# Performance work log

Measured on AMD Instinct MI355X. Metric: run time of the kernel, lower is better.

Reference implementation:

```python
import jax, jax.numpy as jnp
import numpy as np

B, N, D, NS, HID = 256, 1024, 64, 8, 128
ITERS, SINK_ITERS, MESH_ITERS = 3, 8, 4
MESH_LR = 3.0
EPS = 1e-8


def _grid():
    # build_coords with latent_resolution=(32,32): meshgrid('xy'), flattened to [1024,2]
    x = np.linspace(0.0, 1.0, 32)
    xv, yv = np.meshgrid(x, x)
    g = np.stack([xv.reshape(-1), yv.reshape(-1)], axis=-1)
    return jnp.asarray(g, dtype=jnp.float32)


def layer_norm(x, g, b):
    m = jnp.mean(x, axis=-1, keepdims=True)
    v = jnp.var(x, axis=-1, keepdims=True)
    return (x - m) * jax.lax.rsqrt(v + 1e-5) * g + b


def cdist(k, q):
    # Euclidean pairwise distance: k [b,n,d], q [b,s,d] -> [b,n,s]
    d2 = (jnp.sum(k * k, -1)[..., :, None] + jnp.sum(q * q, -1)[..., None, :]
          - 2.0 * jnp.einsum('bnd,bsd->bns', k, q))
    return jnp.sqrt(jnp.maximum(d2, 1e-12))


def sinkhorn(C, a, b, u=None, v=None, n_iters=SINK_ITERS):
    # log-domain Sinkhorn; C [b,n,s], row marginal a [b,n], col marginal b [b,s]
    log_a = jnp.log(a + EPS)
    log_b = jnp.log(b + EPS)
    if u is None:
        u = jnp.zeros_like(a)
    if v is None:
        v = jnp.zeros_like(b)
    K = -C

    def body(carry, _):
        u, v = carry
        u = log_a - jax.scipy.special.logsumexp(K + v[..., None, :], axis=-1)
        v = log_b - jax.scipy.special.logsumexp(K + u[..., :, None], axis=-2)
        return (u, v), None

    (u, v), _ = jax.lax.scan(body, (u, v), None, length=n_iters)
    P = jnp.exp(K + u[..., :, None] + v[..., None, :])
    return P, u, v


def minimize_entropy_of_sinkhorn(C0, a, b, mesh_lr=MESH_LR, n_mesh_iters=MESH_ITERS):
    # MESH: gradient descent on the cost matrix to minimize Sinkhorn plan entropy
    def ent(C):
        P, u, v = sinkhorn(C, a, b)
        H = -jnp.sum(P * jnp.log(P + EPS))
        return H, (u, v)

    C = C0
    u = v = None
    for _ in range(n_mesh_iters):
        (_, (u, v)), g = jax.value_and_grad(ent, has_aux=True)(C)
        C = C - mesh_lr * g
    return C, u, v


def gru_cell(x, h, w_ih, w_hh, b_ih, b_hh):
    gi = x @ w_ih.T + b_ih
    gh = h @ w_hh.T + b_hh
    i_r, i_z, i_n = jnp.split(gi, 3, axis=-1)
    h_r, h_z, h_n = jnp.split(gh, 3, axis=-1)
    r = jax.nn.sigmoid(i_r + h_r)
    z = jax.nn.sigmoid(i_z + h_z)
    n = jnp.tanh(i_n + r * h_n)
    return (1.0 - z) * n + z * h


def setup_inputs() -> dict:
    key = jax.random.key(0)
    ks = jax.random.split(key, 16)
    s = D ** -0.5
    inp = {
        'inputs': jax.random.normal(ks[0], (B, N, D), jnp.float32),
        'noise': jax.random.normal(ks[1], (B, NS, D), jnp.float32),
        'slots_mu': jax.random.normal(ks[2], (1, 1, D), jnp.float32),
        'slots_sigma': jax.random.uniform(ks[3], (1, 1, D), jnp.float32),
        'Wq': jax.random.normal(ks[4], (D, D), jnp.float32) * s,
        'Wk': jax.random.normal(ks[5], (D, D), jnp.float32) * s,
        'Wv': jax.random.normal(ks[6], (D, D), jnp.float32) * s,
        'gru_w_ih': jax.random.normal(ks[7], (3 * D, D), jnp.float32) * s,
        'gru_w_hh': jax.random.normal(ks[8], (3 * D, D), jnp.float32) * s,
        'gru_b_ih': jnp.zeros((3 * D,), jnp.float32),
        'gru_b_hh': jnp.zeros((3 * D,), jnp.float32),
        'fc1_w': jax.random.normal(ks[9], (HID, D), jnp.float32) * s,
        'fc1_b': jnp.zeros((HID,), jnp.float32),
        'fc2_w': jax.random.normal(ks[10], (D, HID), jnp.float32) * (HID ** -0.5),
        'fc2_b': jnp.zeros((D,), jnp.float32),
        'ln_in_g': jnp.ones((D,), jnp.float32), 'ln_in_b': jnp.zeros((D,), jnp.float32),
        'ln_slots_g': jnp.ones((D,), jnp.float32), 'ln_slots_b': jnp.zeros((D,), jnp.float32),
        'ln_ff_g': jnp.ones((D,), jnp.float32), 'ln_ff_b': jnp.zeros((D,), jnp.float32),
        'wi_w': jax.random.normal(ks[11], (1, D), jnp.float32) * s,
        'wi_b': jnp.zeros((1,), jnp.float32),
        'ws_w': jax.random.normal(ks[12], (1, D), jnp.float32) * s,
        'ws_b': jnp.zeros((1,), jnp.float32),
    }
    return inp


def _forward(inputs, noise, slots_mu, slots_sigma, Wq, Wk, Wv,
             gru_w_ih, gru_w_hh, gru_b_ih, gru_b_hh,
             fc1_w, fc1_b, fc2_w, fc2_b,
             ln_in_g, ln_in_b, ln_slots_g, ln_slots_b, ln_ff_g, ln_ff_b,
             wi_w, wi_b, ws_w, ws_b):
    b_s, n, d = inputs.shape
    n_s = NS
    # slots ~ Normal(mu, |sigma|+eps) via reparameterized noise
    slots = slots_mu + (jnp.abs(slots_sigma) + EPS) * noise  # [b, n_s, d]

    x = layer_norm(inputs, ln_in_g, ln_in_b)
    k = x @ Wk.T
    v = x @ Wv.T
    grid = _grid()  # [N, 2]
    a = jax.nn.softmax((x @ wi_w.T + wi_b)[..., 0], axis=-1) * n_s  # [b, n]

    for _ in range(ITERS):
        slots_prev = slots
        s_n = layer_norm(slots, ln_slots_g, ln_slots_b)
        bm = jax.nn.softmax((s_n @ ws_w.T + ws_b)[..., 0], axis=-1) * n_s  # [b, n_s]
        q = s_n @ Wq.T
        C = cdist(k, q)  # [b, n, n_s]
        C, p, qq = minimize_entropy_of_sinkhorn(C, a, bm)
        attn, _, _ = sinkhorn(C, a, bm, u=p, v=qq)
        attn = jnp.transpose(attn, (0, 2, 1))  # [b, n_s, n]
        updates = attn @ v  # [b, n_s, d]
        slot_pos = jnp.einsum('bqk,kd->bqd', attn, grid)  # [b, n_s, 2]
        slots = gru_cell(updates.reshape(b_s * n_s, d),
                         slots_prev.reshape(b_s * n_s, d),
                         gru_w_ih, gru_w_hh, gru_b_ih, gru_b_hh).reshape(b_s, n_s, d)
        slots = slots + (jax.nn.relu(layer_norm(slots, ln_ff_g, ln_ff_b) @ fc1_w.T + fc1_b) @ fc2_w.T + fc2_b)
    return slots, slot_pos.reshape(b_s, n_s, 2), attn


def reference(inputs, noise, slots_mu, slots_sigma, Wq, Wk, Wv,
              gru_w_ih, gru_w_hh, gru_b_ih, gru_b_hh,
              fc1_w, fc1_b, fc2_w, fc2_b,
              ln_in_g, ln_in_b, ln_slots_g, ln_slots_b, ln_ff_g, ln_ff_b,
              wi_w, wi_b, ws_w, ws_b):
    return _forward(inputs, noise, slots_mu, slots_sigma, Wq, Wk, Wv,
                    gru_w_ih, gru_w_hh, gru_b_ih, gru_b_hh,
                    fc1_w, fc1_b, fc2_w, fc2_b,
                    ln_in_g, ln_in_b, ln_slots_g, ln_slots_b, ln_ff_g, ln_ff_b,
                    wi_w, wi_b, ws_w, ws_b)
```

## Files before the change

### kernel.cpp

```cpp
#include <hip/hip_runtime.h>
#include <math.h>

#define NB   256
#define NN   1024
#define ND   64
#define NSL  8
#define NHID 128
#define N_SINK 8
#define N_MESH 4
#define F_LR  3.0f
#define F_EPS 1e-8f

__global__ __launch_bounds__(256) void k_pre(
    const float* __restrict__ inp, const float* __restrict__ Wk,
    const float* __restrict__ lng, const float* __restrict__ lnb,
    const float* __restrict__ wiw, const float* __restrict__ wib,
    float* __restrict__ xout, float* __restrict__ kkout, float* __restrict__ wilog) {
  __shared__ __align__(16) float xs[4][64];
  int wv = threadIdx.x >> 6, ln = threadIdx.x & 63;
  size_t row = (size_t)blockIdx.x * 4 + wv;
  float xi = inp[row * 64 + ln];
  float s1 = xi, s2 = xi * xi;
  #pragma unroll
  for (int m = 32; m >= 1; m >>= 1) { s1 += __shfl_xor(s1, m, 64); s2 += __shfl_xor(s2, m, 64); }
  float mean = s1 * (1.f / 64.f);
  float var  = s2 * (1.f / 64.f) - mean * mean;
  float xn = (xi - mean) * rsqrtf(var + 1e-5f) * lng[ln] + lnb[ln];
  xs[wv][ln] = xn;
  xout[row * 64 + ln] = xn;
  float wl = xn * wiw[ln];
  #pragma unroll
  for (int m = 32; m >= 1; m >>= 1) wl += __shfl_xor(wl, m, 64);
  __syncthreads();
  const float4* w4 = (const float4*)(Wk + ln * 64);
  const float4* x4 = (const float4*)xs[wv];
  float ko = 0.f;
  #pragma unroll
  for (int c = 0; c < 16; ++c) {
    float4 a = w4[c], xv = x4[c];
    ko += a.x * xv.x + a.y * xv.y + a.z * xv.z + a.w * xv.w;
  }
  float kk = ko * ko;
  #pragma unroll
  for (int m = 32; m >= 1; m >>= 1) kk += __shfl_xor(kk, m, 64);
  if (ln == 0) { kkout[row] = kk; wilog[row] = wl + wib[0]; }
}

__global__ __launch_bounds__(1024, 4) void k_mega(
    const float* __restrict__ noise, const float* __restrict__ mu,
    const float* __restrict__ sigma,
    const float* __restrict__ xg, const float* __restrict__ kkg,
    const float* __restrict__ wilogg,
    const float* __restrict__ Wq, const float* __restrict__ Wk,
    const float* __restrict__ Wv,
    const float* __restrict__ wih, const float* __restrict__ whh,
    const float* __restrict__ bih, const float* __restrict__ bhh,
    const float* __restrict__ fc1w, const float* __restrict__ fc1b,
    const float* __restrict__ fc2w, const float* __restrict__ fc2b,
    const float* __restrict__ lns_g, const float* __restrict__ lns_b,
    const float* __restrict__ lnf_g, const float* __restrict__ lnf_b,
    const float* __restrict__ wsw, const float* __restrict__ wsb,
    float* __restrict__ out_slots, float* __restrict__ out_pos,
    float* __restrict__ out_attn) {
  __shared__ __align__(16) float slot_lds[8][64];
  __shared__ __align__(16) float sn[8][64];
  __shared__ __align__(16) float qsh[8][64];
  __shared__ __align__(16) float qs[8][64];
  __shared__ __align__(16) float updl[8][64];
  __shared__ __align__(16) float ys[8][64];
  __shared__ __align__(16) float rs[8][128];
  __shared__ __align__(16) union {
    float uhist[N_SINK][NN];
    float part[16][8][64];
  } U;
  __shared__ __align__(16) float cols[8][NN];
  __shared__ float vbc[8];
  __shared__ float vbarbc[8];
  __shared__ float vhist[N_SINK][8];
  __shared__ float bmv[8], q2s[8], lbs[8];
  __shared__ float redf[16], bcf[1];

  int b = blockIdx.x, tid = threadIdx.x;
  int wv = tid >> 6, ln = tid & 63;

  if (tid < 512) {
    slot_lds[tid >> 6][ln] = mu[ln] + (fabsf(sigma[ln]) + F_EPS) * noise[(size_t)b * 512 + tid];
  }
  float wl = wilogg[(size_t)b * NN + tid];
  float m0 = wl;
  #pragma unroll
  for (int s = 32; s >= 1; s >>= 1) m0 = fmaxf(m0, __shfl_xor(m0, s, 64));
  if (ln == 0) redf[wv] = m0;
  __syncthreads();
  if (tid == 0) { float a = redf[0]; for (int w = 1; w < 16; ++w) a = fmaxf(a, redf[w]); bcf[0] = a; }
  __syncthreads();
  m0 = bcf[0];
  float e0 = __expf(wl - m0), se0 = e0;
  #pragma unroll
  for (int s = 32; s >= 1; s >>= 1) se0 += __shfl_xor(se0, s, 64);
  __syncthreads();
  if (ln == 0) redf[wv] = se0;
  __syncthreads();
  if (tid == 0) { float a = 0.f; for (int w = 0; w < 16; ++w) a += redf[w]; bcf[0] = a; }
  __syncthreads();
  float la = __logf(8.f * e0 / bcf[0] + F_EPS);
  float kk = kkg[(size_t)b * NN + tid];
  const float4* xrow4 = (const float4*)(xg + ((size_t)b * NN + tid) * ND);

  float u = 0.f;

  for (int it = 0; it < 3; ++it) {
    if (wv < 8) {
      float x = slot_lds[wv][ln];
      float s1 = x, s2 = x * x;
      #pragma unroll
      for (int m = 32; m >= 1; m >>= 1) { s1 += __shfl_xor(s1, m, 64); s2 += __shfl_xor(s2, m, 64); }
      float mean = s1 * (1.f / 64.f);
      float var  = s2 * (1.f / 64.f) - mean * mean;
      float xn = (x - mean) * rsqrtf(var + 1e-5f) * lns_g[ln] + lns_b[ln];
      sn[wv][ln] = xn;
      float wlg = xn * wsw[ln];
      #pragma unroll
      for (int m = 32; m >= 1; m >>= 1) wlg += __shfl_xor(wlg, m, 64);
      if (ln == 0) bmv[wv] = wlg + wsb[0];
    }
    __syncthreads();
    if (wv < 8) {
      const float4* w4 = (const float4*)(Wq + ln * 64);
      const float4* x4 = (const float4*)sn[wv];
      float q = 0.f;
      #pragma unroll
      for (int c = 0; c < 16; ++c) {
        float4 a = w4[c], xv = x4[c];
        q += a.x * xv.x + a.y * xv.y + a.z * xv.z + a.w * xv.w;
      }
      qsh[wv][ln] = q;
      float q2 = q * q;
      #pragma unroll
      for (int m = 32; m >= 1; m >>= 1) q2 += __shfl_xor(q2, m, 64);
      if (ln == 0) q2s[wv] = q2;
    }
    if (tid >= 512 && tid < 520) {
      int j = tid - 512;
      float mx = bmv[0];
      #pragma unroll
      for (int jj = 1; jj < 8; ++jj) mx = fmaxf(mx, bmv[jj]);
      float ss = 0.f;
      #pragma unroll
      for (int jj = 0; jj < 8; ++jj) ss += __expf(bmv[jj] - mx);
      lbs[j] = __logf(8.f * __expf(bmv[j] - mx) / ss + F_EPS);
    }
    __syncthreads();
    if (wv < 8) {
      float qt = 0.f;
      for (int o = 0; o < 64; ++o) qt = fmaf(qsh[wv][o], Wk[o * 64 + ln], qt);
      qs[wv][ln] = qt;
    }
    __syncthreads();

    float Know[8];
    {
      float dot[8];
      #pragma unroll
      for (int j = 0; j < 8; ++j) dot[j] = 0.f;
      #pragma unroll 4
      for (int c = 0; c < 16; ++c) {
        float4 xv = xrow4[c];
        #pragma unroll
        for (int j = 0; j < 8; ++j) {
          const float4 qv = *(const float4*)&qs[j][c * 4];
          dot[j] += xv.x * qv.x + xv.y * qv.y + xv.z * qv.z + xv.w * qv.w;
        }
      }
      #pragma unroll
      for (int j = 0; j < 8; ++j) {
        float d2 = kk + q2s[j] - 2.f * dot[j];
        Know[j] = -sqrtf(fmaxf(d2, 1e-12f));
      }
    }
    for (int phase = 0; phase <= N_MESH; ++phase) {
      bool cold = (phase < N_MESH);
      for (int t = 0; t < N_SINK; ++t) {
        bool z0 = cold && (t == 0);
        float c0[8];
        #pragma unroll
        for (int j = 0; j < 8; ++j) c0[j] = Know[j] + (z0 ? 0.f : vbc[j]);
        float mx = c0[0];
        #pragma unroll
        for (int j = 1; j < 8; ++j) mx = fmaxf(mx, c0[j]);
        float se = 0.f;
        #pragma unroll
        for (int j = 0; j < 8; ++j) se += __expf(c0[j] - mx);
        u = la - (mx + __logf(se));
        U.uhist[t][tid] = u;
        #pragma unroll
        for (int j = 0; j < 8; ++j) cols[j][tid] = Know[j] + u;
        __syncthreads();
        if (wv < 8) {
          const float* cp = &cols[wv][ln];
          float M = cp[0];
          #pragma unroll
          for (int k = 1; k < 16; ++k) M = fmaxf(M, cp[k * 64]);
          #pragma unroll
          for (int d = 32; d >= 1; d >>= 1) M = fmaxf(M, __shfl_xor(M, d, 64));
          float S = 0.f;
          #pragma unroll
          for (int k = 0; k < 16; ++k) S += __expf(cp[k * 64] - M);
          #pragma unroll
          for (int d = 32; d >= 1; d >>= 1) S += __shfl_xor(S, d, 64);
          if (ln == 0) {
            float vj = lbs[wv] - (M + __logf(S));
            vbc[wv] = vj; vhist[t][wv] = vj;
          }
        }
        __syncthreads();
      }
      if (phase == N_MESH) break;

      float Kbar[8], ubarT;
      {
        float gsum = 0.f;
        #pragma unroll
        for (int j = 0; j < 8; ++j) {
          float P  = __expf(Know[j] + u + vbc[j]);
          float pe = P + F_EPS;
          float G  = -(__logf(pe) + P / pe);
          float gp = G * P;
          Kbar[j] = gp; gsum += gp;
          cols[j][tid] = gp;
        }
        ubarT = gsum;
      }
      __syncthreads();
      if (wv < 8) {
        const float* cp = &cols[wv][ln];
        float S = 0.f;
        #pragma unroll
        for (int k = 0; k < 16; ++k) S += cp[k * 64];
        #pragma unroll
        for (int d = 32; d >= 1; d >>= 1) S += __shfl_xor(S, d, 64);
        if (ln == 0) vbarbc[wv] = S;
      }
      __syncthreads();
      for (int t = N_SINK - 1; t >= 0; --t) {
        float ut = U.uhist[t][tid];
        float dsum = (t == N_SINK - 1) ? ubarT : 0.f;
        #pragma unroll
        for (int j = 0; j < 8; ++j) {
          float w  = __expf(Know[j] + ut + vhist[t][j] - lbs[j]);
          float vw = vbarbc[j] * w;
          Kbar[j] -= vw; dsum -= vw;
        }
        #pragma unroll
        for (int j = 0; j < 8; ++j) {
          float vprev = (t > 0) ? vhist[t - 1][j] : 0.f;
          float z  = __expf(Know[j] + vprev + ut - la);
          float uz = dsum * z;
          Kbar[j] -= uz;
          cols[j][tid] = uz;
        }
        if (t > 0) {
          __syncthreads();
          if (wv < 8) {
            const float* cp = &cols[wv][ln];
            float S = 0.f;
            #pragma unroll
            for (int k = 0; k < 16; ++k) S += cp[k * 64];
            #pragma unroll
            for (int d = 32; d >= 1; d >>= 1) S += __shfl_xor(S, d, 64);
            if (ln == 0) vbarbc[wv] = -S;
          }
          __syncthreads();
        }
      }
      #pragma unroll
      for (int j = 0; j < 8; ++j) Know[j] -= F_LR * Kbar[j];
    }
    #pragma unroll
    for (int j = 0; j < 8; ++j) {
      float P = __expf(Know[j] + u + vbc[j]);
      cols[j][tid] = P;
      if (it == 2) out_attn[((size_t)b * 8 + j) * NN + tid] = P;
    }
    __syncthreads();

    {
      float acc[8];
      #pragma unroll
      for (int j = 0; j < 8; ++j) acc[j] = 0.f;
      const float* xc = xg + ((size_t)b * NN + wv * 64) * ND + ln;
      #pragma unroll 2
      for (int i0 = 0; i0 < 64; i0 += 4) {
        float x0 = xc[(size_t)(i0 + 0) * 64];
        float x1 = xc[(size_t)(i0 + 1) * 64];
        float x2 = xc[(size_t)(i0 + 2) * 64];
        float x3 = xc[(size_t)(i0 + 3) * 64];
        int ir = wv * 64 + i0;
        #pragma unroll
        for (int j = 0; j < 8; ++j) {
          float4 a = *(const float4*)&cols[j][ir];
          acc[j] += a.x * x0 + a.y * x1 + a.z * x2 + a.w * x3;
        }
      }
      #pragma unroll
      for (int j = 0; j < 8; ++j) U.part[wv][j][ln] = acc[j];
    }
    if (it == 2 && wv < 8) {
      float px = 0.f, py = 0.f;
      #pragma unroll
      for (int k = 0; k < 16; ++k) {
        int i = ln + k * 64;
        float a = cols[wv][i];
        px += a * (float)(i & 31);
        py += a * (float)(i >> 5);
      }
      #pragma unroll
      for (int m = 32; m >= 1; m >>= 1) { px += __shfl_xor(px, m, 64); py += __shfl_xor(py, m, 64); }
      if (ln == 0) {
        out_pos[(b * 8 + wv) * 2 + 0] = px * (1.f / 31.f);
        out_pos[(b * 8 + wv) * 2 + 1] = py * (1.f / 31.f);
      }
    }
    __syncthreads();
    if (wv < 8) {
      float s = 0.f;
      #pragma unroll
      for (int w = 0; w < 16; ++w) s += U.part[w][wv][ln];
      updl[wv][ln] = s;
    }
    __syncthreads();
    if (wv < 8) {
      const float4* w4 = (const float4*)(Wv + ln * 64);
      const float4* u4 = (const float4*)updl[wv];
      float updv = 0.f;
      #pragma unroll
      for (int c = 0; c < 16; ++c) {
        float4 uv = u4[c], wvv = w4[c];
        updv += uv.x * wvv.x + uv.y * wvv.y + uv.z * wvv.z + uv.w * wvv.w;
      }
      sn[wv][ln] = updv;
    }
    __syncthreads();

    float hn = 0.f;
    if (wv < 8) {
      float h = slot_lds[wv][ln];
      float gi0 = bih[ln], gi1 = bih[64 + ln], gi2 = bih[128 + ln];
      float gh0 = bhh[ln], gh1 = bhh[64 + ln], gh2 = bhh[128 + ln];
      const float4* x4 = (const float4*)sn[wv];
      const float4* h4 = (const float4*)slot_lds[wv];
      const float4* wi0 = (const float4*)(wih + (size_t)ln * 64);
      const float4* wi1 = (const float4*)(wih + (size_t)(64 + ln) * 64);
      const float4* wi2 = (const float4*)(wih + (size_t)(128 + ln) * 64);
      const float4* wh0 = (const float4*)(whh + (size_t)ln * 64);
      const float4* wh1 = (const float4*)(whh + (size_t)(64 + ln) * 64);
      const float4* wh2 = (const float4*)(whh + (size_t)(128 + ln) * 64);
      #pragma unroll 4
      for (int c = 0; c < 16; ++c) {
        float4 xv = x4[c], hv = h4[c], a;
        a = wi0[c]; gi0 += xv.x * a.x + xv.y * a.y + xv.z * a.z + xv.w * a.w;
        a = wi1[c]; gi1 += xv.x * a.x + xv.y * a.y + xv.z * a.z + xv.w * a.w;
        a = wi2[c]; gi2 += xv.x * a.x + xv.y * a.y + xv.z * a.z + xv.w * a.w;
        a = wh0[c]; gh0 += hv.x * a.x + hv.y * a.y + hv.z * a.z + hv.w * a.w;
        a = wh1[c]; gh1 += hv.x * a.x + hv.y * a.y + hv.z * a.z + hv.w * a.w;
        a = wh2[c]; gh2 += hv.x * a.x + hv.y * a.y + hv.z * a.z + hv.w * a.w;
      }
      float r = 1.f / (1.f + expf(-(gi0 + gh0)));
      float z = 1.f / (1.f + expf(-(gi1 + gh1)));
      float n = tanhf(gi2 + r * gh2);
      hn = (1.f - z) * n + z * h;
      float s1 = hn, s2 = hn * hn;
      #pragma unroll
      for (int m = 32; m >= 1; m >>= 1) { s1 += __shfl_xor(s1, m, 64); s2 += __shfl_xor(s2, m, 64); }
      float mean = s1 * (1.f / 64.f);
      float var  = s2 * (1.f / 64.f) - mean * mean;
      ys[wv][ln] = (hn - mean) * rsqrtf(var + 1e-5f) * lnf_g[ln] + lnf_b[ln];
    }
    __syncthreads();
    if (wv < 8) {
      float a0 = fc1b[ln], a1 = fc1b[64 + ln];
      const float4* y4 = (const float4*)ys[wv];
      const float4* f0 = (const float4*)(fc1w + (size_t)ln * 64);
      const float4* f1 = (const float4*)(fc1w + (size_t)(64 + ln) * 64);
      #pragma unroll 4
      for (int c = 0; c < 16; ++c) {
        float4 yv = y4[c], a = f0[c], bb = f1[c];
        a0 += yv.x * a.x + yv.y * a.y + yv.z * a.z + yv.w * a.w;
        a1 += yv.x * bb.x + yv.y * bb.y + yv.z * bb.z + yv.w * bb.w;
      }
      rs[wv][ln] = fmaxf(a0, 0.f);
      rs[wv][64 + ln] = fmaxf(a1, 0.f);
    }
    __syncthreads();
    if (wv < 8) {
      float o = fc2b[ln];
      const float4* r4 = (const float4*)rs[wv];
      const float4* f2 = (const float4*)(fc2w + (size_t)ln * 128);
      #pragma unroll 4
      for (int c = 0; c < 32; ++c) {
        float4 rv = r4[c], a = f2[c];
        o += rv.x * a.x + rv.y * a.y + rv.z * a.z + rv.w * a.w;
      }
      slot_lds[wv][ln] = hn + o;
    }
    __syncthreads();
  }
  if (tid < 512) out_slots[(size_t)b * 512 + tid] = slot_lds[tid >> 6][ln];
}

extern "C" void kernel_launch(void* const* d_in, const int* in_sizes, int n_in,
                              void* d_out, int out_size, void* d_ws, size_t ws_size,
                              hipStream_t stream) {
  const float* inputs = (const float*)d_in[0];
  const float* noise  = (const float*)d_in[1];
  const float* mu     = (const float*)d_in[2];
  const float* sigma  = (const float*)d_in[3];
  const float* Wq     = (const float*)d_in[4];
  const float* Wk     = (const float*)d_in[5];
  const float* Wv     = (const float*)d_in[6];
  const float* gwih   = (const float*)d_in[7];
  const float* gwhh   = (const float*)d_in[8];
  const float* gbih   = (const float*)d_in[9];
  const float* gbhh   = (const float*)d_in[10];
  const float* fc1w   = (const float*)d_in[11];
  const float* fc1b   = (const float*)d_in[12];
  const float* fc2w   = (const float*)d_in[13];
  const float* fc2b   = (const float*)d_in[14];
  const float* lnin_g = (const float*)d_in[15];
  const float* lnin_b = (const float*)d_in[16];
  const float* lns_g  = (const float*)d_in[17];
  const float* lns_b  = (const float*)d_in[18];
  const float* lnf_g  = (const float*)d_in[19];
  const float* lnf_b  = (const float*)d_in[20];
  const float* wi_w   = (const float*)d_in[21];
  const float* wi_b   = (const float*)d_in[22];
  const float* ws_w   = (const float*)d_in[23];
  const float* ws_b   = (const float*)d_in[24];

  float* out       = (float*)d_out;
  float* out_slots = out;
  float* out_pos   = out + NB * NSL * ND;
  float* out_attn  = out_pos + NB * NSL * 2;

  float* p = (float*)d_ws;
  float* xbuf  = p; p += (size_t)NB * NN * ND;
  float* kkbuf = p; p += (size_t)NB * NN;
  float* wilog = p; p += (size_t)NB * NN;

  k_pre<<<(NB * NN) / 4, 256, 0, stream>>>(inputs, Wk, lnin_g, lnin_b, wi_w, wi_b,
                                           xbuf, kkbuf, wilog);
  k_mega<<<NB, 1024, 0, stream>>>(noise, mu, sigma, xbuf, kkbuf, wilog,
                                  Wq, Wk, Wv, gwih, gwhh, gbih, gbhh,
                                  fc1w, fc1b, fc2w, fc2b,
                                  lns_g, lns_b, lnf_g, lnf_b, ws_w, ws_b,
                                  out_slots, out_pos, out_attn);
}
```

Measured before the change: 1.330 ms.

## Keep cost matrix in LDS and recompute column terms instead of staging cols

The per-thread Know[8] register array becomes a shared-memory cost matrix, and the separate cols staging buffer is removed. Column reductions now recompute their terms (the exp and log expressions) directly from know, uhist, dsum and la held in LDS, which also drops one barrier in the mesh backward step. The launch-bounds occupancy hint is relaxed and several unroll factors are reduced to lower register pressure. The cost is extra transcendental recomputation in the wave-limited column reductions and LDS reads in place of register reads.

After: 1.317 ms. Within noise of the previous version (-1.0%).

```diff
diff --git a/kernel.cpp b/kernel.cpp
--- a/kernel.cpp
+++ b/kernel.cpp
@@ -46,7 +46,7 @@
   if (ln == 0) { kkout[row] = kk; wilog[row] = wl + wib[0]; }
 }
 
-__global__ __launch_bounds__(1024, 4) void k_mega(
+__global__ __launch_bounds__(1024) void k_mega(
     const float* __restrict__ noise, const float* __restrict__ mu,
     const float* __restrict__ sigma,
     const float* __restrict__ xg, const float* __restrict__ kkg,
@@ -62,6 +62,13 @@
     const float* __restrict__ wsw, const float* __restrict__ wsb,
     float* __restrict__ out_slots, float* __restrict__ out_pos,
     float* __restrict__ out_attn) {
+  __shared__ __align__(16) float know[8][NN];
+  __shared__ __align__(16) union {
+    float uhist[N_SINK][NN];
+    float part[16][8][64];
+  } U;
+  __shared__ __align__(16) float dsb[NN];
+  __shared__ __align__(16) float la_lds[NN];
   __shared__ __align__(16) float slot_lds[8][64];
   __shared__ __align__(16) float sn[8][64];
   __shared__ __align__(16) float qsh[8][64];
@@ -69,11 +76,6 @@
   __shared__ __align__(16) float updl[8][64];
   __shared__ __align__(16) float ys[8][64];
   __shared__ __align__(16) float rs[8][128];
-  __shared__ __align__(16) union {
-    float uhist[N_SINK][NN];
-    float part[16][8][64];
-  } U;
-  __shared__ __align__(16) float cols[8][NN];
   __shared__ float vbc[8];
   __shared__ float vbarbc[8];
   __shared__ float vhist[N_SINK][8];
@@ -104,6 +106,7 @@
   if (tid == 0) { float a = 0.f; for (int w = 0; w < 16; ++w) a += redf[w]; bcf[0] = a; }
   __syncthreads();
   float la = __logf(8.f * e0 / bcf[0] + F_EPS);
+  la_lds[tid] = la;
   float kk = kkg[(size_t)b * NN + tid];
   const float4* xrow4 = (const float4*)(xg + ((size_t)b * NN + tid) * ND);
 
@@ -158,7 +161,6 @@
     }
     __syncthreads();
 
-    float Know[8];
     {
       float dot[8];
       #pragma unroll
@@ -175,37 +177,37 @@
       #pragma unroll
       for (int j = 0; j < 8; ++j) {
         float d2 = kk + q2s[j] - 2.f * dot[j];
-        Know[j] = -sqrtf(fmaxf(d2, 1e-12f));
+        know[j][tid] = -sqrtf(fmaxf(d2, 1e-12f));
       }
     }
     for (int phase = 0; phase <= N_MESH; ++phase) {
       bool cold = (phase < N_MESH);
       for (int t = 0; t < N_SINK; ++t) {
         bool z0 = cold && (t == 0);
-        float c0[8];
-        #pragma unroll
-        for (int j = 0; j < 8; ++j) c0[j] = Know[j] + (z0 ? 0.f : vbc[j]);
-        float mx = c0[0];
-        #pragma unroll
-        for (int j = 1; j < 8; ++j) mx = fmaxf(mx, c0[j]);
+        float kv[8];
+        #pragma unroll
+        for (int j = 0; j < 8; ++j) kv[j] = know[j][tid] + (z0 ? 0.f : vbc[j]);
+        float mx = kv[0];
+        #pragma unroll
+        for (int j = 1; j < 8; ++j) mx = fmaxf(mx, kv[j]);
         float se = 0.f;
         #pragma unroll
-        for (int j = 0; j < 8; ++j) se += __expf(c0[j] - mx);
+        for (int j = 0; j < 8; ++j) se += __expf(kv[j] - mx);
         u = la - (mx + __logf(se));
         U.uhist[t][tid] = u;
-        #pragma unroll
-        for (int j = 0; j < 8; ++j) cols[j][tid] = Know[j] + u;
         __syncthreads();
         if (wv < 8) {
-          const float* cp = &cols[wv][ln];
-          float M = cp[0];
+          float tv[16];
           #pragma unroll
-          for (int k = 1; k < 16; ++k) M = fmaxf(M, cp[k * 64]);
+          for (int k = 0; k < 16; ++k) tv[k] = know[wv][ln + k * 64] + U.uhist[t][ln + k * 64];
+          float M = tv[0];
+          #pragma unroll
+          for (int k = 1; k < 16; ++k) M = fmaxf(M, tv[k]);
           #pragma unroll
           for (int d = 32; d >= 1; d >>= 1) M = fmaxf(M, __shfl_xor(M, d, 64));
           float S = 0.f;
           #pragma unroll
-          for (int k = 0; k < 16; ++k) S += __expf(cp[k * 64] - M);
+          for (int k = 0; k < 16; ++k) S += __expf(tv[k] - M);
           #pragma unroll
           for (int d = 32; d >= 1; d >>= 1) S += __shfl_xor(S, d, 64);
           if (ln == 0) {
@@ -222,21 +224,23 @@
         float gsum = 0.f;
         #pragma unroll
         for (int j = 0; j < 8; ++j) {
-          float P  = __expf(Know[j] + u + vbc[j]);
+          float P  = __expf(know[j][tid] + u + vbc[j]);
           float pe = P + F_EPS;
-          float G  = -(__logf(pe) + P / pe);
-          float gp = G * P;
+          float gp = -(__logf(pe) + P / pe) * P;
           Kbar[j] = gp; gsum += gp;
-          cols[j][tid] = gp;
         }
         ubarT = gsum;
       }
-      __syncthreads();
       if (wv < 8) {
-        const float* cp = &cols[wv][ln];
+        float vj = vbc[wv];
         float S = 0.f;
         #pragma unroll
-        for (int k = 0; k < 16; ++k) S += cp[k * 64];
+        for (int k = 0; k < 16; ++k) {
+          int i = ln + k * 64;
+          float P  = __expf(know[wv][i] + U.uhist[N_SINK - 1][i] + vj);
+          float pe = P + F_EPS;
+          S += -(__logf(pe) + P / pe) * P;
+        }
         #pragma unroll
         for (int d = 32; d >= 1; d >>= 1) S += __shfl_xor(S, d, 64);
         if (ln == 0) vbarbc[wv] = S;
@@ -247,25 +251,28 @@
         float dsum = (t == N_SINK - 1) ? ubarT : 0.f;
         #pragma unroll
         for (int j = 0; j < 8; ++j) {
-          float w  = __expf(Know[j] + ut + vhist[t][j] - lbs[j]);
+          float w  = __expf(know[j][tid] + ut + vhist[t][j] - lbs[j]);
           float vw = vbarbc[j] * w;
           Kbar[j] -= vw; dsum -= vw;
         }
         #pragma unroll
         for (int j = 0; j < 8; ++j) {
           float vprev = (t > 0) ? vhist[t - 1][j] : 0.f;
-          float z  = __expf(Know[j] + vprev + ut - la);
-          float uz = dsum * z;
-          Kbar[j] -= uz;
-          cols[j][tid] = uz;
+          float z  = __expf(know[j][tid] + vprev + ut - la);
+          Kbar[j] -= dsum * z;
         }
         if (t > 0) {
+          dsb[tid] = dsum;
           __syncthreads();
           if (wv < 8) {
-            const float* cp = &cols[wv][ln];
+            float vp = vhist[t - 1][wv];
             float S = 0.f;
             #pragma unroll
-            for (int k = 0; k < 16; ++k) S += cp[k * 64];
+            for (int k = 0; k < 16; ++k) {
+              int i = ln + k * 64;
+              float z = __expf(know[wv][i] + vp + U.uhist[t][i] - la_lds[i]);
+              S += dsb[i] * z;
+            }
             #pragma unroll
             for (int d = 32; d >= 1; d >>= 1) S += __shfl_xor(S, d, 64);
             if (ln == 0) vbarbc[wv] = -S;
@@ -274,12 +281,12 @@
         }
       }
       #pragma unroll
-      for (int j = 0; j < 8; ++j) Know[j] -= F_LR * Kbar[j];
+      for (int j = 0; j < 8; ++j) know[j][tid] -= F_LR * Kbar[j];
     }
     #pragma unroll
     for (int j = 0; j < 8; ++j) {
-      float P = __expf(Know[j] + u + vbc[j]);
-      cols[j][tid] = P;
+      float P = __expf(know[j][tid] + u + vbc[j]);
+      know[j][tid] = P;
       if (it == 2) out_attn[((size_t)b * 8 + j) * NN + tid] = P;
     }
     __syncthreads();
@@ -298,7 +305,7 @@
         int ir = wv * 64 + i0;
         #pragma unroll
         for (int j = 0; j < 8; ++j) {
-          float4 a = *(const float4*)&cols[j][ir];
+          float4 a = *(const float4*)&know[j][ir];
           acc[j] += a.x * x0 + a.y * x1 + a.z * x2 + a.w * x3;
         }
       }
@@ -310,7 +317,7 @@
       #pragma unroll
       for (int k = 0; k < 16; ++k) {
         int i = ln + k * 64;
-        float a = cols[wv][i];
+        float a = know[wv][i];
         px += a * (float)(i & 31);
         py += a * (float)(i >> 5);
       }
@@ -355,7 +362,7 @@
       const float4* wh0 = (const float4*)(whh + (size_t)ln * 64);
       const float4* wh1 = (const float4*)(whh + (size_t)(64 + ln) * 64);
       const float4* wh2 = (const float4*)(whh + (size_t)(128 + ln) * 64);
-      #pragma unroll 4
+      #pragma unroll 2
       for (int c = 0; c < 16; ++c) {
         float4 xv = x4[c], hv = h4[c], a;
         a = wi0[c]; gi0 += xv.x * a.x + xv.y * a.y + xv.z * a.z + xv.w * a.w;
@@ -382,7 +389,7 @@
       const float4* y4 = (const float4*)ys[wv];
       const float4* f0 = (const float4*)(fc1w + (size_t)ln * 64);
       const float4* f1 = (const float4*)(fc1w + (size_t)(64 + ln) * 64);
-      #pragma unroll 4
+      #pragma unroll 2
       for (int c = 0; c < 16; ++c) {
         float4 yv = y4[c], a = f0[c], bb = f1[c];
         a0 += yv.x * a.x + yv.y * a.y + yv.z * a.z + yv.w * a.w;
@@ -396,7 +403,7 @@
       float o = fc2b[ln];
       const float4* r4 = (const float4*)rs[wv];
       const float4* f2 = (const float4*)(fc2w + (size_t)ln * 128);
-      #pragma unroll 4
+      #pragma unroll 2
       for (int c = 0; c < 32; ++c) {
         float4 rv = r4[c], a = f2[c];
         o += rv.x * a.x + rv.y * a.y + rv.z * a.z + rv.w * a.w;
```
